# Kernel optimization log

Measured on AMD Instinct MI355X. Metric: run time of the kernel, lower is better.

The kernel has to match this reference:

```python
import jax, jax.numpy as jnp
import numpy as np

N_NODES = 100000
N_EDGES = 1600000
IN_FEAT = 256
HIDDEN = 64
N_CLASSES = 16


def gcn_conv(x, edge_index, W, b):
    """PyG GCNConv: add self-loops, symmetric normalization, linear+aggregate."""
    n = x.shape[0]
    src, dst = edge_index[0], edge_index[1]
    loops = jnp.arange(n, dtype=src.dtype)
    src = jnp.concatenate([src, loops])
    dst = jnp.concatenate([dst, loops])
    # in-degree on graph with self-loops
    deg = jax.ops.segment_sum(jnp.ones(src.shape[0], dtype=x.dtype), dst, num_segments=n)
    dinv = jnp.where(deg > 0, jax.lax.rsqrt(deg), 0.0)
    h = x @ W                                  # [N, out]
    norm = dinv[src] * dinv[dst]               # [E+N]
    msg = h[src] * norm[:, None]                # gather + scale (memory-bound)
    out = jax.ops.segment_sum(msg, dst, num_segments=n)  # scatter-add
    return out + b


def setup_inputs() -> dict:
    key = jax.random.key(0)
    ks = jax.random.split(key, 5)
    x = jax.random.normal(ks[0], (N_NODES, IN_FEAT), dtype=jnp.float32)
    edge_index = jax.random.randint(ks[1], (2, N_EDGES), 0, N_NODES, dtype=jnp.int64)
    W1 = jax.random.normal(ks[2], (IN_FEAT, HIDDEN), dtype=jnp.float32) * (1.0 / np.sqrt(IN_FEAT))
    b1 = jnp.zeros((HIDDEN,), dtype=jnp.float32)
    W2 = jax.random.normal(ks[3], (HIDDEN, N_CLASSES), dtype=jnp.float32) * (1.0 / np.sqrt(HIDDEN))
    b2 = jnp.zeros((N_CLASSES,), dtype=jnp.float32)
    return {"x": x, "edge_index": edge_index, "W1": W1, "b1": b1, "W2": W2, "b2": b2}


def reference(x, edge_index, W1, b1, W2, b2):
    h = gcn_conv(x, edge_index, W1, b1)
    h = jax.nn.relu(h)
    # dropout p=0.5 is identity in eval mode (training=False)
    out = gcn_conv(h, edge_index, W2, b2)
    return out
```

## Files before the change

### kernel.cpp

```cpp
#include <hip/hip_runtime.h>

#define NN 100000
#define NE 1600000
#define FIN 256
#define FH 64
#define FC 16

#define NPB 512
#define NBKT ((NN + NPB - 1) / NPB)
#define NBLK 256
#define CHUNK (NE / NBLK)
#define CAP 12288
#define NB_GEMM1 ((NN + 127) / 128)

typedef int v2i __attribute__((ext_vector_type(2)));
typedef int v4i __attribute__((ext_vector_type(4)));
typedef short s16x8 __attribute__((ext_vector_type(8)));
typedef float f32x4 __attribute__((ext_vector_type(4)));
typedef _Float16 h16x8 __attribute__((ext_vector_type(8)));
typedef _Float16 h16x4 __attribute__((ext_vector_type(4)));

__device__ __forceinline__ float4 fma4(float4 v, float w, float4 a) {
    a.x = fmaf(v.x, w, a.x); a.y = fmaf(v.y, w, a.y);
    a.z = fmaf(v.z, w, a.z); a.w = fmaf(v.w, w, a.w);
    return a;
}
__device__ __forceinline__ float4 add4(float4 a, float4 v) {
    a.x += v.x; a.y += v.y; a.z += v.z; a.w += v.w;
    return a;
}
__device__ __forceinline__ float4 xor_add4(float4 r, int m) {
    r.x += __shfl_xor(r.x, m, 64); r.y += __shfl_xor(r.y, m, 64);
    r.z += __shfl_xor(r.z, m, 64); r.w += __shfl_xor(r.w, m, 64);
    return r;
}

__device__ __forceinline__ unsigned short bf16rne(float f) {
    unsigned u = __float_as_uint(f);
    u += 0x7FFFu + ((u >> 16) & 1u);
    return (unsigned short)(u >> 16);
}
__device__ __forceinline__ void split8(const float* f, s16x8& hi, s16x8& lo) {
    #pragma unroll
    for (int i = 0; i < 8; i++) {
        unsigned u = __float_as_uint(f[i]);
        unsigned short h = (unsigned short)((u + 0x7FFFu + ((u >> 16) & 1u)) >> 16);
        float l = f[i] - __uint_as_float((unsigned)h << 16);
        unsigned ul = __float_as_uint(l);
        hi[i] = (short)h;
        lo[i] = (short)((ul + 0x7FFFu + ((ul >> 16) & 1u)) >> 16);
    }
}
__device__ __forceinline__ int is64(const int* __restrict__ ei) {
    return (ei[1] == 0) & (ei[3] == 0) & (ei[5] == 0) & (ei[7] == 0);
}

__global__ __launch_bounds__(256) void histprep_k(const int* __restrict__ ei,
                                                  const float* __restrict__ W,
                                                  unsigned short* __restrict__ Whi,
                                                  unsigned short* __restrict__ Wlo,
                                                  int* __restrict__ cnt) {
    const int b = blockIdx.x, t = threadIdx.x;
    if (b < 8) {
        int slot = b * 256 + t;
        int l = slot & 63;
        int c = (slot >> 6) & 3;
        int s = slot >> 8;
        int k0 = s * 32 + (l >> 4) * 8;
        int col = c * 16 + (l & 15);
        #pragma unroll
        for (int i = 0; i < 8; i++) {
            float f = W[(k0 + i) * FH + col];
            unsigned short h = bf16rne(f);
            float lres = f - __uint_as_float((unsigned)h << 16);
            Whi[slot * 8 + i] = h;
            Wlo[slot * 8 + i] = bf16rne(lres);
        }
        return;
    }
    __shared__ int hist[NBKT];
    const int blk = b - 8;
    for (int j = t; j < NBKT; j += 256) hist[j] = 0;
    __syncthreads();
    int f = is64(ei);
    int base = blk * CHUNK;
    if (f) {
        for (int i = t; i < CHUNK; i += 256) {
            v2i p = *(const v2i*)&ei[2 * (NE + base + i)];
            atomicAdd(&hist[p.x >> 9], 1);
        }
    } else {
        for (int i = t; i < CHUNK; i += 256) {
            int d = ei[NE + base + i];
            atomicAdd(&hist[d >> 9], 1);
        }
    }
    __syncthreads();
    for (int j = t; j < NBKT; j += 256) cnt[j * NBLK + blk] = hist[j];
}

__global__ __launch_bounds__(1024) void scanoff_k(int* __restrict__ cnt,
                                                  int* __restrict__ bucketBase) {
    __shared__ int s[1024];
    const int t = threadIdx.x;
    const int SEG = (NBKT * NBLK) / 1024;
    int base = t * SEG;
    int sum = 0;
    for (int i = 0; i < SEG; i++) sum += cnt[base + i];
    s[t] = sum; __syncthreads();
    for (int off = 1; off < 1024; off <<= 1) {
        int u = (t >= off) ? s[t - off] : 0;
        __syncthreads();
        s[t] += u;
        __syncthreads();
    }
    int run = s[t] - sum;
    for (int i = 0; i < SEG; i++) {
        int g = base + i;
        int v = cnt[g];
        cnt[g] = run;
        if ((g & (NBLK - 1)) == 0) bucketBase[g / NBLK] = run;
        run += v;
    }
    if (t == 0) bucketBase[NBKT] = NE;
}

__global__ __launch_bounds__(256) void scat_k(const int* __restrict__ ei,
                                              const int* __restrict__ cnt,
                                              int* __restrict__ sorted) {
    __shared__ int offl[NBKT];
    const int t = threadIdx.x, blk = blockIdx.x;
    for (int j = t; j < NBKT; j += 256) offl[j] = cnt[j * NBLK + blk];
    __syncthreads();
    int f = is64(ei);
    int base = blk * CHUNK;
    if (f) {
        for (int i = t; i < CHUNK; i += 256) {
            int e = base + i;
            v2i ps = *(const v2i*)&ei[2 * e];
            v2i pd = *(const v2i*)&ei[2 * (NE + e)];
            int s = ps.x, d = pd.x;
            int pos = atomicAdd(&offl[d >> 9], 1);
            sorted[pos] = s | ((d & (NPB - 1)) << 17);
        }
    } else {
        for (int i = t; i < CHUNK; i += 256) {
            int e = base + i;
            int s = ei[e], d = ei[NE + e];
            int pos = atomicAdd(&offl[d >> 9], 1);
            sorted[pos] = s | ((d & (NPB - 1)) << 17);
        }
    }
}

__global__ __launch_bounds__(256) void bucket_k(const int* __restrict__ sorted,
                                                const int* __restrict__ bucketBase,
                                                int* __restrict__ csr,
                                                int* __restrict__ row_start,
                                                float* __restrict__ dinv) {
    __shared__ int stash[CAP];
    __shared__ int hist[NPB];
    __shared__ int startl[NPB];
    __shared__ int cursor[NPB];
    __shared__ int ss[256];
    const int t = threadIdx.x, b = blockIdx.x;
    const int nb0 = b * NPB;
    const int ncnt = (NN - nb0 < NPB) ? (NN - nb0) : NPB;
    const int ebase = bucketBase[b];
    const int ecnt = bucketBase[b + 1] - ebase;

    hist[t] = 0; hist[t + 256] = 0;
    __syncthreads();
    for (int i = t; i < ecnt; i += 256) {
        int v = sorted[ebase + i];
        if (i < CAP) stash[i] = v;
        atomicAdd(&hist[v >> 17], 1);
    }
    __syncthreads();
    int a = hist[2 * t], c = hist[2 * t + 1];
    int p = a + c;
    ss[t] = p; __syncthreads();
    for (int off = 1; off < 256; off <<= 1) {
        int u = (t >= off) ? ss[t - off] : 0;
        __syncthreads();
        ss[t] += u;
        __syncthreads();
    }
    int ex = ss[t] - p;
    startl[2 * t] = ex;       startl[2 * t + 1] = ex + a;
    cursor[2 * t] = ex;       cursor[2 * t + 1] = ex + a;
    __syncthreads();
    for (int j = t; j < ncnt; j += 256) {
        row_start[nb0 + j] = ebase + startl[j];
        dinv[nb0 + j] = rsqrtf((float)(hist[j] + 1));
    }
    if (b == 0 && t == 0) row_start[NN] = NE;
    for (int i = t; i < ecnt; i += 256) {
        int v = (i < CAP) ? stash[i] : sorted[ebase + i];
        int dl = v >> 17;
        int r = atomicAdd(&cursor[dl], 1);
        csr[ebase + r] = v & 0x1FFFF;
    }
}

__global__ __launch_bounds__(256, 4) void gemm1_k(const float* __restrict__ x,
                                                  const unsigned short* __restrict__ Whi,
                                                  const unsigned short* __restrict__ Wlo,
                                                  const float* __restrict__ dinv,
                                                  _Float16* __restrict__ h1h) {
    const int t = threadIdx.x;
    const int lane = t & 63;
    const int wid = t >> 6;
    const int mb = blockIdx.x * 128 + wid * 32;
    const int lr = lane & 15;
    const int lk = (lane >> 4) * 8;

    int ra0 = mb + lr;
    int ra1 = mb + 16 + lr;
    const float* pa0 = x + (size_t)(ra0 < NN ? ra0 : NN - 1) * FIN + lk;
    const float* pa1 = x + (size_t)(ra1 < NN ? ra1 : NN - 1) * FIN + lk;

    f32x4 acc[2][4] = {};

    for (int s = 0; s < 8; s++) {
        float fa0[8], fa1[8];
        float4 q;
        q = *(const float4*)(pa0 + s * 32);
        fa0[0] = q.x; fa0[1] = q.y; fa0[2] = q.z; fa0[3] = q.w;
        q = *(const float4*)(pa0 + s * 32 + 4);
        fa0[4] = q.x; fa0[5] = q.y; fa0[6] = q.z; fa0[7] = q.w;
        q = *(const float4*)(pa1 + s * 32);
        fa1[0] = q.x; fa1[1] = q.y; fa1[2] = q.z; fa1[3] = q.w;
        q = *(const float4*)(pa1 + s * 32 + 4);
        fa1[4] = q.x; fa1[5] = q.y; fa1[6] = q.z; fa1[7] = q.w;

        s16x8 a0h, a0l, a1h, a1l;
        split8(fa0, a0h, a0l);
        split8(fa1, a1h, a1l);

        #pragma unroll
        for (int c = 0; c < 4; c++) {
            s16x8 wh = *(const s16x8*)&Whi[((s * 4 + c) * 64 + lane) * 8];
            s16x8 wl = *(const s16x8*)&Wlo[((s * 4 + c) * 64 + lane) * 8];
            acc[0][c] = __builtin_amdgcn_mfma_f32_16x16x32_bf16(a0h, wh, acc[0][c], 0, 0, 0);
            acc[0][c] = __builtin_amdgcn_mfma_f32_16x16x32_bf16(a0l, wh, acc[0][c], 0, 0, 0);
            acc[0][c] = __builtin_amdgcn_mfma_f32_16x16x32_bf16(a0h, wl, acc[0][c], 0, 0, 0);
            acc[1][c] = __builtin_amdgcn_mfma_f32_16x16x32_bf16(a1h, wh, acc[1][c], 0, 0, 0);
            acc[1][c] = __builtin_amdgcn_mfma_f32_16x16x32_bf16(a1l, wh, acc[1][c], 0, 0, 0);
            acc[1][c] = __builtin_amdgcn_mfma_f32_16x16x32_bf16(a1h, wl, acc[1][c], 0, 0, 0);
        }
    }
    #pragma unroll
    for (int r = 0; r < 2; r++) {
        int rowb = mb + 16 * r + (lane >> 4) * 4;
        #pragma unroll
        for (int v = 0; v < 4; v++) {
            int row = rowb + v;
            if (row < NN) {
                float dn = dinv[row];
                #pragma unroll
                for (int c = 0; c < 4; c++)
                    h1h[(size_t)row * FH + 16 * c + lr] = (_Float16)(acc[r][c][v] * dn);
            }
        }
    }
}

__global__ __launch_bounds__(256) void agg1g_k(const int* __restrict__ csr,
                                               const int* __restrict__ row_start,
                                               const _Float16* __restrict__ h1h,
                                               const float* __restrict__ dinv,
                                               const float* __restrict__ b1,
                                               const float* __restrict__ W2,
                                               _Float16* __restrict__ h2h) {
    __shared__ float sW2[FH * FC];
    __shared__ float sp[4][FH];
    const int t = threadIdx.x;
    #pragma unroll
    for (int i = 0; i < 4; i++) sW2[t + 256 * i] = W2[t + 256 * i];
    __syncthreads();

    const int wid = t >> 6;
    const int n = blockIdx.x * 4 + wid;
    const int lane = t & 63;
    if (n >= NN) return;
    const int sg = lane >> 3;
    const int fl = lane & 7;
    const h16x8* hp = (const h16x8*)h1h;
    int s0 = row_start[n], s1 = row_start[n + 1];
    float aA[8] = {}, aB[8] = {};
    for (int j0 = s0; j0 < s1; j0 += 64) {
        int idx = j0 + lane;
        int sl = (idx < s1) ? csr[idx] : 0;
        int cnt = s1 - j0; if (cnt > 64) cnt = 64;
        int j = 0;
        for (; j + 16 <= cnt; j += 16) {
            int eA = __shfl(sl, j + sg, 64);
            int eB = __shfl(sl, j + 8 + sg, 64);
            h16x8 vA = hp[eA * 8 + fl];
            h16x8 vB = hp[eB * 8 + fl];
            #pragma unroll
            for (int i = 0; i < 8; i++) { aA[i] += (float)vA[i]; aB[i] += (float)vB[i]; }
        }
        if (j + 8 <= cnt) {
            int eA = __shfl(sl, j + sg, 64);
            h16x8 vA = hp[eA * 8 + fl];
            #pragma unroll
            for (int i = 0; i < 8; i++) aA[i] += (float)vA[i];
            j += 8;
        }
        int rem = cnt - j;
        if (rem > 0) {
            int jj = j + (sg < rem ? sg : 0);
            int eA = __shfl(sl, jj, 64);
            float w = (sg < rem) ? 1.f : 0.f;
            h16x8 vA = hp[eA * 8 + fl];
            #pragma unroll
            for (int i = 0; i < 8; i++) aA[i] = fmaf(w, (float)vA[i], aA[i]);
        }
    }
    #pragma unroll
    for (int i = 0; i < 8; i++) {
        float r = aA[i] + aB[i];
        r += __shfl_xor(r, 8, 64);
        r += __shfl_xor(r, 16, 64);
        r += __shfl_xor(r, 32, 64);
        aA[i] = r;
    }
    float dn = dinv[n];
    if (sg == 0) {
        h16x8 sv = hp[n * 8 + fl];
        float4 p0, p1;
        float4 bq0 = *(const float4*)&b1[fl * 8];
        float4 bq1 = *(const float4*)&b1[fl * 8 + 4];
        p0.x = fmaxf(fmaf(aA[0] + (float)sv[0], dn, bq0.x), 0.f);
        p0.y = fmaxf(fmaf(aA[1] + (float)sv[1], dn, bq0.y), 0.f);
        p0.z = fmaxf(fmaf(aA[2] + (float)sv[2], dn, bq0.z), 0.f);
        p0.w = fmaxf(fmaf(aA[3] + (float)sv[3], dn, bq0.w), 0.f);
        p1.x = fmaxf(fmaf(aA[4] + (float)sv[4], dn, bq1.x), 0.f);
        p1.y = fmaxf(fmaf(aA[5] + (float)sv[5], dn, bq1.y), 0.f);
        p1.z = fmaxf(fmaf(aA[6] + (float)sv[6], dn, bq1.z), 0.f);
        p1.w = fmaxf(fmaf(aA[7] + (float)sv[7], dn, bq1.w), 0.f);
        *(float4*)&sp[wid][fl * 8] = p0;
        *(float4*)&sp[wid][fl * 8 + 4] = p1;
    }
    __builtin_amdgcn_s_waitcnt(0);
    if (lane < FC) {
        float o = 0.f;
        #pragma unroll 8
        for (int k = 0; k < FH; k++)
            o = fmaf(sp[wid][k], sW2[k * FC + lane], o);
        h2h[n * FC + lane] = (_Float16)(o * dn);
    }
}

__global__ __launch_bounds__(256) void agg2_k(const int* __restrict__ csr,
                                              const int* __restrict__ row_start,
                                              const _Float16* __restrict__ h2h,
                                              const float* __restrict__ dinv,
                                              const float* __restrict__ b2,
                                              float* __restrict__ out) {
    const int t = threadIdx.x;
    int n = blockIdx.x * 16 + (t >> 4);
    int l16 = t & 15;
    int base = t & 48;
    int q = (t >> 2) & 3;
    int c = t & 3;
    if (n >= NN) return;
    const h16x4* hp = (const h16x4*)h2h;
    int s0 = row_start[n], s1 = row_start[n + 1];
    float4 A = make_float4(0.f, 0.f, 0.f, 0.f);
    float4 B = make_float4(0.f, 0.f, 0.f, 0.f);
    float4 C = make_float4(0.f, 0.f, 0.f, 0.f);
    float4 D = make_float4(0.f, 0.f, 0.f, 0.f);
    for (int j0 = s0; j0 < s1; j0 += 16) {
        int idx = j0 + l16;
        int sl = (idx < s1) ? csr[idx] : 0;
        int cnt = s1 - j0; if (cnt > 16) cnt = 16;
        int j = 0;
        if (j + 16 <= cnt) {
            int eA = __shfl(sl, base + j + q, 64);
            int eB = __shfl(sl, base + j + 4 + q, 64);
            int eC = __shfl(sl, base + j + 8 + q, 64);
            int eD = __shfl(sl, base + j + 12 + q, 64);
            h16x4 vA = hp[eA * 4 + c];
            h16x4 vB = hp[eB * 4 + c];
            h16x4 vC = hp[eC * 4 + c];
            h16x4 vD = hp[eD * 4 + c];
            A.x += (float)vA[0]; A.y += (float)vA[1]; A.z += (float)vA[2]; A.w += (float)vA[3];
            B.x += (float)vB[0]; B.y += (float)vB[1]; B.z += (float)vB[2]; B.w += (float)vB[3];
            C.x += (float)vC[0]; C.y += (float)vC[1]; C.z += (float)vC[2]; C.w += (float)vC[3];
            D.x += (float)vD[0]; D.y += (float)vD[1]; D.z += (float)vD[2]; D.w += (float)vD[3];
            j += 16;
        }
        if (j + 8 <= cnt) {
            int eA = __shfl(sl, base + j + q, 64);
            int eB = __shfl(sl, base + j + 4 + q, 64);
            h16x4 vA = hp[eA * 4 + c];
            h16x4 vB = hp[eB * 4 + c];
            A.x += (float)vA[0]; A.y += (float)vA[1]; A.z += (float)vA[2]; A.w += (float)vA[3];
            B.x += (float)vB[0]; B.y += (float)vB[1]; B.z += (float)vB[2]; B.w += (float)vB[3];
            j += 8;
        }
        if (j + 4 <= cnt) {
            int eA = __shfl(sl, base + j + q, 64);
            h16x4 vA = hp[eA * 4 + c];
            A.x += (float)vA[0]; A.y += (float)vA[1]; A.z += (float)vA[2]; A.w += (float)vA[3];
            j += 4;
        }
        int rem = cnt - j;
        if (rem > 0) {
            int jj = base + j + (q < rem ? q : 0);
            int eA = __shfl(sl, jj, 64);
            float wA = (q < rem) ? 1.f : 0.f;
            h16x4 vA = hp[eA * 4 + c];
            float4 vf = make_float4((float)vA[0], (float)vA[1], (float)vA[2], (float)vA[3]);
            A = fma4(vf, wA, A);
        }
    }
    float4 r = add4(add4(A, B), add4(C, D));
    r = xor_add4(r, 4);
    r = xor_add4(r, 8);
    if (q == 0) {
        float dn = dinv[n];
        h16x4 sv = hp[n * 4 + c];
        float4 bq = *(const float4*)&b2[c * 4];
        float4 p;
        p.x = fmaf(r.x + (float)sv[0], dn, bq.x);
        p.y = fmaf(r.y + (float)sv[1], dn, bq.y);
        p.z = fmaf(r.z + (float)sv[2], dn, bq.z);
        p.w = fmaf(r.w + (float)sv[3], dn, bq.w);
        *(float4*)&out[n * FC + c * 4] = p;
    }
}

extern "C" void kernel_launch(void* const* d_in, const int* in_sizes, int n_in,
                              void* d_out, int out_size, void* d_ws, size_t ws_size,
                              hipStream_t stream) {
    const float* x  = (const float*)d_in[0];
    const int*   ei = (const int*)d_in[1];
    const float* W1 = (const float*)d_in[2];
    const float* b1 = (const float*)d_in[3];
    const float* W2 = (const float*)d_in[4];
    const float* b2 = (const float*)d_in[5];
    float* out = (float*)d_out;

    char* ws = (char*)d_ws;
    int*   row_start  = (int*)(ws + 0);
    float* dinv       = (float*)(ws + 512ull * 1024);
    int*   bucketBase = (int*)(ws + 960ull * 1024);
    unsigned short* Whi = (unsigned short*)(ws + 1024ull * 1024);
    unsigned short* Wlo = (unsigned short*)(ws + 1088ull * 1024);
    int*   cnt        = (int*)(ws + 1152ull * 1024);
    int*   csr        = (int*)(ws + 2048ull * 1024);
    int*   sorted     = (int*)(ws + 9216ull * 1024);
    _Float16* h1h     = (_Float16*)(ws + 16384ull * 1024);
    _Float16* h2h     = (_Float16*)(ws + 30720ull * 1024);

    histprep_k<<<8 + NBLK, 256, 0, stream>>>(ei, W1, Whi, Wlo, cnt);
    scanoff_k<<<1, 1024, 0, stream>>>(cnt, bucketBase);
    scat_k<<<NBLK, 256, 0, stream>>>(ei, cnt, sorted);
    bucket_k<<<NBKT, 256, 0, stream>>>(sorted, bucketBase, csr, row_start, dinv);
    gemm1_k<<<NB_GEMM1, 256, 0, stream>>>(x, Whi, Wlo, dinv, h1h);
    agg1g_k<<<(NN + 3) / 4, 256, 0, stream>>>(csr, row_start, h1h, dinv, b1, W2, h2h);
    agg2_k<<<(NN + 15) / 16, 256, 0, stream>>>(csr, row_start, h2h, dinv, b2, out);
}
```

Measured before the change: 388.4 us.

## Fuse edge scatter with GEMM1, locally sort scatter, and accumulate gathers in fp16

The edge scatter and the first GEMM now run as one launch with disjoint block roles, so the index work overlaps the x@W1 compute. The dinv row scaling moves out of the GEMM into bucket_k, which rescales h1 in place once degrees are known. The scatter now stages edges in shared memory sorted by bucket so the global writes are more contiguous. The aggregation kernels accumulate gathered fp16 vectors in fp16 packed adds per 64-edge chunk before converting to fp32. This cuts conversion ALU work but loses precision. The fused kernel uses much more shared memory, which may lower GEMM occupancy, and bucket_k adds an extra read-modify-write pass over h1.

```diff
diff --git a/kernel.cpp b/kernel.cpp
--- a/kernel.cpp
+++ b/kernel.cpp
@@ -20,11 +20,6 @@
 typedef _Float16 h16x8 __attribute__((ext_vector_type(8)));
 typedef _Float16 h16x4 __attribute__((ext_vector_type(4)));
 
-__device__ __forceinline__ float4 fma4(float4 v, float w, float4 a) {
-    a.x = fmaf(v.x, w, a.x); a.y = fmaf(v.y, w, a.y);
-    a.z = fmaf(v.z, w, a.z); a.w = fmaf(v.w, w, a.w);
-    return a;
-}
 __device__ __forceinline__ float4 add4(float4 a, float4 v) {
     a.x += v.x; a.y += v.y; a.z += v.z; a.w += v.w;
     return a;
@@ -33,6 +28,18 @@
     r.x += __shfl_xor(r.x, m, 64); r.y += __shfl_xor(r.y, m, 64);
     r.z += __shfl_xor(r.z, m, 64); r.w += __shfl_xor(r.w, m, 64);
     return r;
+}
+__device__ __forceinline__ h16x8 hz8() {
+    h16x8 p;
+    #pragma unroll
+    for (int i = 0; i < 8; i++) p[i] = (_Float16)0.0f;
+    return p;
+}
+__device__ __forceinline__ h16x4 hz4() {
+    h16x4 p;
+    #pragma unroll
+    for (int i = 0; i < 4; i++) p[i] = (_Float16)0.0f;
+    return p;
 }
 
 __device__ __forceinline__ unsigned short bf16rne(float f) {
@@ -125,93 +132,78 @@
     if (t == 0) bucketBase[NBKT] = NE;
 }
 
-__global__ __launch_bounds__(256) void scat_k(const int* __restrict__ ei,
-                                              const int* __restrict__ cnt,
-                                              int* __restrict__ sorted) {
-    __shared__ int offl[NBKT];
-    const int t = threadIdx.x, blk = blockIdx.x;
-    for (int j = t; j < NBKT; j += 256) offl[j] = cnt[j * NBLK + blk];
-    __syncthreads();
-    int f = is64(ei);
-    int base = blk * CHUNK;
-    if (f) {
+__global__ __launch_bounds__(256, 4) void scatgemm_k(const int* __restrict__ ei,
+                                                     const int* __restrict__ cnt,
+                                                     int* __restrict__ sorted,
+                                                     const float* __restrict__ x,
+                                                     const unsigned short* __restrict__ Whi,
+                                                     const unsigned short* __restrict__ Wlo,
+                                                     _Float16* __restrict__ h1h) {
+    __shared__ int stash[CHUNK];
+    __shared__ unsigned short bkt[CHUNK];
+    __shared__ int lhist[NBKT];
+    __shared__ int lstart[NBKT];
+    __shared__ int lcur[NBKT];
+    __shared__ int sred[256];
+    const int b = blockIdx.x, t = threadIdx.x;
+    if (b >= NB_GEMM1) {
+        const int blk = b - NB_GEMM1;
+        for (int j = t; j < NBKT; j += 256) lhist[j] = 0;
+        __syncthreads();
+        int f = is64(ei);
+        int base = blk * CHUNK;
+        if (f) {
+            for (int i = t; i < CHUNK; i += 256) {
+                v2i p = *(const v2i*)&ei[2 * (NE + base + i)];
+                atomicAdd(&lhist[p.x >> 9], 1);
+            }
+        } else {
+            for (int i = t; i < CHUNK; i += 256)
+                atomicAdd(&lhist[ei[NE + base + i] >> 9], 1);
+        }
+        __syncthreads();
+        int v = (t < NBKT) ? lhist[t] : 0;
+        sred[t] = v; __syncthreads();
+        for (int off = 1; off < 256; off <<= 1) {
+            int u = (t >= off) ? sred[t - off] : 0;
+            __syncthreads();
+            sred[t] += u;
+            __syncthreads();
+        }
+        if (t < NBKT) { lstart[t] = sred[t] - v; lcur[t] = sred[t] - v; }
+        __syncthreads();
+        if (f) {
+            for (int i = t; i < CHUNK; i += 256) {
+                int e = base + i;
+                v2i ps = *(const v2i*)&ei[2 * e];
+                v2i pd = *(const v2i*)&ei[2 * (NE + e)];
+                int s = ps.x, d = pd.x;
+                int bk = d >> 9;
+                int pos = atomicAdd(&lcur[bk], 1);
+                stash[pos] = s | ((d & (NPB - 1)) << 17);
+                bkt[pos] = (unsigned short)bk;
+            }
+        } else {
+            for (int i = t; i < CHUNK; i += 256) {
+                int e = base + i;
+                int s = ei[e], d = ei[NE + e];
+                int bk = d >> 9;
+                int pos = atomicAdd(&lcur[bk], 1);
+                stash[pos] = s | ((d & (NPB - 1)) << 17);
+                bkt[pos] = (unsigned short)bk;
+            }
+        }
+        __syncthreads();
         for (int i = t; i < CHUNK; i += 256) {
-            int e = base + i;
-            v2i ps = *(const v2i*)&ei[2 * e];
-            v2i pd = *(const v2i*)&ei[2 * (NE + e)];
-            int s = ps.x, d = pd.x;
-            int pos = atomicAdd(&offl[d >> 9], 1);
-            sorted[pos] = s | ((d & (NPB - 1)) << 17);
-        }
-    } else {
-        for (int i = t; i < CHUNK; i += 256) {
-            int e = base + i;
-            int s = ei[e], d = ei[NE + e];
-            int pos = atomicAdd(&offl[d >> 9], 1);
-            sorted[pos] = s | ((d & (NPB - 1)) << 17);
-        }
-    }
-}
-
-__global__ __launch_bounds__(256) void bucket_k(const int* __restrict__ sorted,
-                                                const int* __restrict__ bucketBase,
-                                                int* __restrict__ csr,
-                                                int* __restrict__ row_start,
-                                                float* __restrict__ dinv) {
-    __shared__ int stash[CAP];
-    __shared__ int hist[NPB];
-    __shared__ int startl[NPB];
-    __shared__ int cursor[NPB];
-    __shared__ int ss[256];
-    const int t = threadIdx.x, b = blockIdx.x;
-    const int nb0 = b * NPB;
-    const int ncnt = (NN - nb0 < NPB) ? (NN - nb0) : NPB;
-    const int ebase = bucketBase[b];
-    const int ecnt = bucketBase[b + 1] - ebase;
-
-    hist[t] = 0; hist[t + 256] = 0;
-    __syncthreads();
-    for (int i = t; i < ecnt; i += 256) {
-        int v = sorted[ebase + i];
-        if (i < CAP) stash[i] = v;
-        atomicAdd(&hist[v >> 17], 1);
-    }
-    __syncthreads();
-    int a = hist[2 * t], c = hist[2 * t + 1];
-    int p = a + c;
-    ss[t] = p; __syncthreads();
-    for (int off = 1; off < 256; off <<= 1) {
-        int u = (t >= off) ? ss[t - off] : 0;
-        __syncthreads();
-        ss[t] += u;
-        __syncthreads();
-    }
-    int ex = ss[t] - p;
-    startl[2 * t] = ex;       startl[2 * t + 1] = ex + a;
-    cursor[2 * t] = ex;       cursor[2 * t + 1] = ex + a;
-    __syncthreads();
-    for (int j = t; j < ncnt; j += 256) {
-        row_start[nb0 + j] = ebase + startl[j];
-        dinv[nb0 + j] = rsqrtf((float)(hist[j] + 1));
-    }
-    if (b == 0 && t == 0) row_start[NN] = NE;
-    for (int i = t; i < ecnt; i += 256) {
-        int v = (i < CAP) ? stash[i] : sorted[ebase + i];
-        int dl = v >> 17;
-        int r = atomicAdd(&cursor[dl], 1);
-        csr[ebase + r] = v & 0x1FFFF;
-    }
-}
-
-__global__ __launch_bounds__(256, 4) void gemm1_k(const float* __restrict__ x,
-                                                  const unsigned short* __restrict__ Whi,
-                                                  const unsigned short* __restrict__ Wlo,
-                                                  const float* __restrict__ dinv,
-                                                  _Float16* __restrict__ h1h) {
-    const int t = threadIdx.x;
+            int bk = bkt[i];
+            int g = cnt[bk * NBLK + blk] + (i - lstart[bk]);
+            sorted[g] = stash[i];
+        }
+        return;
+    }
     const int lane = t & 63;
     const int wid = t >> 6;
-    const int mb = blockIdx.x * 128 + wid * 32;
+    const int mb = b * 128 + wid * 32;
     const int lr = lane & 15;
     const int lk = (lane >> 4) * 8;
 
@@ -257,12 +249,71 @@
         for (int v = 0; v < 4; v++) {
             int row = rowb + v;
             if (row < NN) {
-                float dn = dinv[row];
                 #pragma unroll
                 for (int c = 0; c < 4; c++)
-                    h1h[(size_t)row * FH + 16 * c + lr] = (_Float16)(acc[r][c][v] * dn);
+                    h1h[(size_t)row * FH + 16 * c + lr] = (_Float16)acc[r][c][v];
             }
         }
+    }
+}
+
+__global__ __launch_bounds__(256) void bucket_k(const int* __restrict__ sorted,
+                                                const int* __restrict__ bucketBase,
+                                                int* __restrict__ csr,
+                                                int* __restrict__ row_start,
+                                                float* __restrict__ dinv,
+                                                _Float16* __restrict__ h1h) {
+    __shared__ int stash[CAP];
+    __shared__ int hist[NPB];
+    __shared__ int startl[NPB];
+    __shared__ int cursor[NPB];
+    __shared__ int ss[256];
+    const int t = threadIdx.x, b = blockIdx.x;
+    const int nb0 = b * NPB;
+    const int ncnt = (NN - nb0 < NPB) ? (NN - nb0) : NPB;
+    const int ebase = bucketBase[b];
+    const int ecnt = bucketBase[b + 1] - ebase;
+
+    hist[t] = 0; hist[t + 256] = 0;
+    __syncthreads();
+    for (int i = t; i < ecnt; i += 256) {
+        int v = sorted[ebase + i];
+        if (i < CAP) stash[i] = v;
+        atomicAdd(&hist[v >> 17], 1);
+    }
+    __syncthreads();
+    int a = hist[2 * t], c = hist[2 * t + 1];
+    int p = a + c;
+    ss[t] = p; __syncthreads();
+    for (int off = 1; off < 256; off <<= 1) {
+        int u = (t >= off) ? ss[t - off] : 0;
+        __syncthreads();
+        ss[t] += u;
+        __syncthreads();
+    }
+    int ex = ss[t] - p;
+    startl[2 * t] = ex;       startl[2 * t + 1] = ex + a;
+    cursor[2 * t] = ex;       cursor[2 * t + 1] = ex + a;
+    __syncthreads();
+    for (int j = t; j < ncnt; j += 256) {
+        row_start[nb0 + j] = ebase + startl[j];
+        dinv[nb0 + j] = rsqrtf((float)(hist[j] + 1));
+    }
+    if (b == 0 && t == 0) row_start[NN] = NE;
+    for (int i = t; i < ecnt; i += 256) {
+        int v = (i < CAP) ? stash[i] : sorted[ebase + i];
+        int dl = v >> 17;
+        int r = atomicAdd(&cursor[dl], 1);
+        csr[ebase + r] = v & 0x1FFFF;
+    }
+    h16x8* hp = (h16x8*)h1h;
+    for (int q = t; q < ncnt * 8; q += 256) {
+        int rl = q >> 3;
+        _Float16 dvh = (_Float16)rsqrtf((float)(hist[rl] + 1));
+        h16x8 v = hp[(size_t)(nb0 + rl) * 8 + (q & 7)];
+        #pragma unroll
+        for (int i = 0; i < 8; i++) v[i] = v[i] * dvh;
+        hp[(size_t)(nb0 + rl) * 8 + (q & 7)] = v;
     }
 }
 
@@ -288,44 +339,42 @@
     const int fl = lane & 7;
     const h16x8* hp = (const h16x8*)h1h;
     int s0 = row_start[n], s1 = row_start[n + 1];
-    float aA[8] = {}, aB[8] = {};
+    float facc[8] = {};
     for (int j0 = s0; j0 < s1; j0 += 64) {
         int idx = j0 + lane;
         int sl = (idx < s1) ? csr[idx] : 0;
         int cnt = s1 - j0; if (cnt > 64) cnt = 64;
+        h16x8 pA = hz8(), pB = hz8();
         int j = 0;
         for (; j + 16 <= cnt; j += 16) {
             int eA = __shfl(sl, j + sg, 64);
             int eB = __shfl(sl, j + 8 + sg, 64);
-            h16x8 vA = hp[eA * 8 + fl];
-            h16x8 vB = hp[eB * 8 + fl];
-            #pragma unroll
-            for (int i = 0; i < 8; i++) { aA[i] += (float)vA[i]; aB[i] += (float)vB[i]; }
+            pA += hp[eA * 8 + fl];
+            pB += hp[eB * 8 + fl];
         }
         if (j + 8 <= cnt) {
             int eA = __shfl(sl, j + sg, 64);
-            h16x8 vA = hp[eA * 8 + fl];
-            #pragma unroll
-            for (int i = 0; i < 8; i++) aA[i] += (float)vA[i];
+            pA += hp[eA * 8 + fl];
             j += 8;
         }
         int rem = cnt - j;
         if (rem > 0) {
             int jj = j + (sg < rem ? sg : 0);
             int eA = __shfl(sl, jj, 64);
-            float w = (sg < rem) ? 1.f : 0.f;
-            h16x8 vA = hp[eA * 8 + fl];
-            #pragma unroll
-            for (int i = 0; i < 8; i++) aA[i] = fmaf(w, (float)vA[i], aA[i]);
-        }
+            h16x8 v = hp[eA * 8 + fl];
+            if (sg < rem) pB += v;
+        }
+        #pragma unroll
+        for (int i = 0; i < 8; i++)
+            facc[i] += (float)pA[i] + (float)pB[i];
     }
     #pragma unroll
     for (int i = 0; i < 8; i++) {
-        float r = aA[i] + aB[i];
+        float r = facc[i];
         r += __shfl_xor(r, 8, 64);
         r += __shfl_xor(r, 16, 64);
         r += __shfl_xor(r, 32, 64);
-        aA[i] = r;
+        facc[i] = r;
     }
     float dn = dinv[n];
     if (sg == 0) {
@@ -333,14 +382,14 @@
         float4 p0, p1;
         float4 bq0 = *(const float4*)&b1[fl * 8];
         float4 bq1 = *(const float4*)&b1[fl * 8 + 4];
-        p0.x = fmaxf(fmaf(aA[0] + (float)sv[0], dn, bq0.x), 0.f);
-        p0.y = fmaxf(fmaf(aA[1] + (float)sv[1], dn, bq0.y), 0.f);
-        p0.z = fmaxf(fmaf(aA[2] + (float)sv[2], dn, bq0.z), 0.f);
-        p0.w = fmaxf(fmaf(aA[3] + (float)sv[3], dn, bq0.w), 0.f);
-        p1.x = fmaxf(fmaf(aA[4] + (float)sv[4], dn, bq1.x), 0.f);
-        p1.y = fmaxf(fmaf(aA[5] + (float)sv[5], dn, bq1.y), 0.f);
-        p1.z = fmaxf(fmaf(aA[6] + (float)sv[6], dn, bq1.z), 0.f);
-        p1.w = fmaxf(fmaf(aA[7] + (float)sv[7], dn, bq1.w), 0.f);
+        p0.x = fmaxf(fmaf(facc[0] + (float)sv[0], dn, bq0.x), 0.f);
+        p0.y = fmaxf(fmaf(facc[1] + (float)sv[1], dn, bq0.y), 0.f);
+        p0.z = fmaxf(fmaf(facc[2] + (float)sv[2], dn, bq0.z), 0.f);
+        p0.w = fmaxf(fmaf(facc[3] + (float)sv[3], dn, bq0.w), 0.f);
+        p1.x = fmaxf(fmaf(facc[4] + (float)sv[4], dn, bq1.x), 0.f);
+        p1.y = fmaxf(fmaf(facc[5] + (float)sv[5], dn, bq1.y), 0.f);
+        p1.z = fmaxf(fmaf(facc[6] + (float)sv[6], dn, bq1.z), 0.f);
+        p1.w = fmaxf(fmaf(facc[7] + (float)sv[7], dn, bq1.w), 0.f);
         *(float4*)&sp[wid][fl * 8] = p0;
         *(float4*)&sp[wid][fl * 8 + 4] = p1;
     }
@@ -369,10 +418,7 @@
     if (n >= NN) return;
     const h16x4* hp = (const h16x4*)h2h;
     int s0 = row_start[n], s1 = row_start[n + 1];
-    float4 A = make_float4(0.f, 0.f, 0.f, 0.f);
-    float4 B = make_float4(0.f, 0.f, 0.f, 0.f);
-    float4 C = make_float4(0.f, 0.f, 0.f, 0.f);
-    float4 D = make_float4(0.f, 0.f, 0.f, 0.f);
+    h16x4 pA = hz4(), pB = hz4(), pC = hz4(), pD = hz4();
     for (int j0 = s0; j0 < s1; j0 += 16) {
         int idx = j0 + l16;
         int sl = (idx < s1) ? csr[idx] : 0;
@@ -383,43 +429,37 @@
             int eB = __shfl(sl, base + j + 4 + q, 64);
             int eC = __shfl(sl, base + j + 8 + q, 64);
             int eD = __shfl(sl, base + j + 12 + q, 64);
-            h16x4 vA = hp[eA * 4 + c];
-            h16x4 vB = hp[eB * 4 + c];
-            h16x4 vC = hp[eC * 4 + c];
-            h16x4 vD = hp[eD * 4 + c];
-            A.x += (float)vA[0]; A.y += (float)vA[1]; A.z += (float)vA[2]; A.w += (float)vA[3];
-            B.x += (float)vB[0]; B.y += (float)vB[1]; B.z += (float)vB[2]; B.w += (float)vB[3];
-            C.x += (float)vC[0]; C.y += (float)vC[1]; C.z += (float)vC[2]; C.w += (float)vC[3];
-            D.x += (float)vD[0]; D.y += (float)vD[1]; D.z += (float)vD[2]; D.w += (float)vD[3];
+            pA += hp[eA * 4 + c];
+            pB += hp[eB * 4 + c];
+            pC += hp[eC * 4 + c];
+            pD += hp[eD * 4 + c];
             j += 16;
         }
         if (j + 8 <= cnt) {
             int eA = __shfl(sl, base + j + q, 64);
             int eB = __shfl(sl, base + j + 4 + q, 64);
-            h16x4 vA = hp[eA * 4 + c];
-            h16x4 vB = hp[eB * 4 + c];
-            A.x += (float)vA[0]; A.y += (float)vA[1]; A.z += (float)vA[2]; A.w += (float)vA[3];
-            B.x += (float)vB[0]; B.y += (float)vB[1]; B.z += (float)vB[2]; B.w += (float)vB[3];
+            pA += hp[eA * 4 + c];
+            pB += hp[eB * 4 + c];
             j += 8;
         }
         if (j + 4 <= cnt) {
             int eA = __shfl(sl, base + j + q, 64);
-            h16x4 vA = hp[eA * 4 + c];
-            A.x += (float)vA[0]; A.y += (float)vA[1]; A.z += (float)vA[2]; A.w += (float)vA[3];
+            pA += hp[eA * 4 + c];
             j += 4;
         }
         int rem = cnt - j;
         if (rem > 0) {
             int jj = base + j + (q < rem ? q : 0);
             int eA = __shfl(sl, jj, 64);
-            float wA = (q < rem) ? 1.f : 0.f;
-            h16x4 vA = hp[eA * 4 + c];
-            float4 vf = make_float4((float)vA[0], (float)vA[1], (float)vA[2], (float)vA[3]);
-            A = fma4(vf, wA, A);
-        }
-    }
-    float4 r = add4(add4(A, B), add4(C, D));
-    r = xor_add4(r, 4);
+            h16x4 v = hp[eA * 4 + c];
+            if (q < rem) pD += v;
+        }
+    }
+    float4 A = make_float4((float)pA[0] + (float)pB[0] + (float)pC[0] + (float)pD[0],
+                           (float)pA[1] + (float)pB[1] + (float)pC[1] + (float)pD[1],
+                           (float)pA[2] + (float)pB[2] + (float)pC[2] + (float)pD[2],
+                           (float)pA[3] + (float)pB[3] + (float)pC[3] + (float)pD[3]);
+    float4 r = xor_add4(A, 4);
     r = xor_add4(r, 8);
     if (q == 0) {
         float dn = dinv[n];
@@ -459,9 +499,8 @@
 
     histprep_k<<<8 + NBLK, 256, 0, stream>>>(ei, W1, Whi, Wlo, cnt);
     scanoff_k<<<1, 1024, 0, stream>>>(cnt, bucketBase);
-    scat_k<<<NBLK, 256, 0, stream>>>(ei, cnt, sorted);
-    bucket_k<<<NBKT, 256, 0, stream>>>(sorted, bucketBase, csr, row_start, dinv);
-    gemm1_k<<<NB_GEMM1, 256, 0, stream>>>(x, Whi, Wlo, dinv, h1h);
+    scatgemm_k<<<NB_GEMM1 + NBLK, 256, 0, stream>>>(ei, cnt, sorted, x, Whi, Wlo, h1h);
+    bucket_k<<<NBKT, 256, 0, stream>>>(sorted, bucketBase, csr, row_start, dinv, h1h);
     agg1g_k<<<(NN + 3) / 4, 256, 0, stream>>>(csr, row_start, h1h, dinv, b1, W2, h2h);
     agg2_k<<<(NN + 15) / 16, 256, 0, stream>>>(csr, row_start, h2h, dinv, b2, out);
 }
```

Measured after the change: 388.5 us. About the same (+0.0%).
